# Optimization experiments

Measured on AMD Instinct MI355X. Metric: run time of the kernel, lower is better.

Reference implementation:

```python
import jax, jax.numpy as jnp
import numpy as np

UNITS = 1024
D_MODEL = 1024
H = 16
DK = 64
DV = 64
M = 128
B = 4
S = 1024


def setup_inputs() -> dict:
    key = jax.random.key(0)
    ks = jax.random.split(key, 12)
    s = 1.0 / np.sqrt(D_MODEL)
    inp = {
        "queries": jax.random.normal(ks[0], (B, S, D_MODEL), jnp.float32),
        "keys": jax.random.normal(ks[1], (B, S, D_MODEL), jnp.float32),
        "values": jax.random.normal(ks[2], (B, S, D_MODEL), jnp.float32),
        "Wq": jax.random.normal(ks[3], (D_MODEL, H * DK), jnp.float32) * s,
        "bq": jnp.zeros((H * DK,), jnp.float32),
        "Wk": jax.random.normal(ks[4], (D_MODEL, H * DK), jnp.float32) * s,
        "bk": jnp.zeros((H * DK,), jnp.float32),
        "Wv": jax.random.normal(ks[5], (D_MODEL, H * DV), jnp.float32) * s,
        "bv": jnp.zeros((H * DV,), jnp.float32),
        "Wo": jax.random.normal(ks[6], (H * DV, UNITS), jnp.float32) * (1.0 / np.sqrt(H * DV)),
        "bo": jnp.zeros((UNITS,), jnp.float32),
        "mk": jax.random.normal(ks[7], (1, M, H * DK), jnp.float32) * 0.1,
        "mv": jax.random.normal(ks[8], (1, M, H * DV), jnp.float32) * 0.1,
        "h": H,
    }
    return inp


def reference(queries, keys, values, Wq, bq, Wk, bk, Wv, bv, Wo, bo, mk, mv, h):
    Bq, Sq, _ = queries.shape
    m = mk.shape[1]
    dk = Wk.shape[1] // h
    dv = Wv.shape[1] // h
    scale_m = jnp.sqrt(jnp.asarray(m, queries.dtype))

    # Q projection: [B, h, Sq, dk]
    q = (queries @ Wq + bq).reshape(Bq, Sq, h, dk).transpose(0, 2, 1, 3)

    # K/V projections with m learned memory slots concatenated on the seq axis
    k_flat = jnp.concatenate(
        [keys @ Wk + bk, scale_m * jnp.broadcast_to(mk, (Bq, m, h * dk))], axis=1
    )  # [B, Sk+m, h*dk]
    v_flat = jnp.concatenate(
        [values @ Wv + bv, scale_m * jnp.broadcast_to(mv, (Bq, m, h * dv))], axis=1
    )  # [B, Sk+m, h*dv]
    Skm = k_flat.shape[1]
    k = k_flat.reshape(Bq, Skm, h, dk).transpose(0, 2, 1, 3)  # [B, h, Sk+m, dk]
    v = v_flat.reshape(Bq, Skm, h, dv).transpose(0, 2, 1, 3)  # [B, h, Sk+m, dv]

    # Scaled dot-product attention over sequence + memory slots
    scores = jnp.einsum("bhqd,bhkd->bhqk", q, k) / jnp.sqrt(jnp.asarray(dk, q.dtype))
    attn = jax.nn.softmax(scores, axis=-1)  # [B, h, Sq, Sk+m]
    out = jnp.einsum("bhqk,bhkd->bhqd", attn, v)  # [B, h, Sq, dv]
    out = out.transpose(0, 2, 1, 3).reshape(Bq, Sq, h * dv)
    return out @ Wo + bo
```

## Files before the change

kernel.cpp:

```cpp
#include <hip/hip_runtime.h>

typedef __attribute__((ext_vector_type(8))) __bf16 bf16x8;
typedef __attribute__((ext_vector_type(4))) float f32x4;

#define DEVINL __device__ __forceinline__

constexpr int BZ = 4;
constexpr int SEQ = 1024;
constexpr int DMODEL = 1024;
constexpr int NH = 16;
constexpr int HD = 64;
constexpr int MSLOT = 128;
constexpr int NT = BZ * SEQ;
constexpr int SKM = SEQ + MSLOT;
constexpr int VT_LD = BZ * SKM;
constexpr float SCALE_M = 11.313708498984761f;
constexpr float SCEXP = 0.18033688011112042f;
constexpr size_t OF_QIN  = 0;
constexpr size_t OF_KIN  = OF_QIN  + (size_t)NT * DMODEL;
constexpr size_t OF_VIN  = OF_KIN  + (size_t)NT * DMODEL;
constexpr size_t OF_WQT  = OF_VIN  + (size_t)NT * DMODEL;
constexpr size_t OF_WKT  = OF_WQT  + (size_t)DMODEL * DMODEL;
constexpr size_t OF_WVT  = OF_WKT  + (size_t)DMODEL * DMODEL;
constexpr size_t OF_WOT  = OF_WVT  + (size_t)DMODEL * DMODEL;
constexpr size_t OF_QB   = OF_WOT  + (size_t)DMODEL * DMODEL;
constexpr size_t OF_KPR  = OF_QB   + (size_t)NT * DMODEL;
constexpr size_t OF_KMEM = OF_KPR  + (size_t)NT * DMODEL;
constexpr size_t OF_VTG  = OF_KMEM + (size_t)MSLOT * DMODEL;
constexpr size_t OF_AOUT = OF_VTG  + (size_t)DMODEL * VT_LD;

DEVINL unsigned short f2bf(float f) {
  union { float f; unsigned u; } v; v.f = f;
  unsigned r = v.u + 0x7FFF + ((v.u >> 16) & 1);
  return (unsigned short)(r >> 16);
}

#if __has_builtin(__builtin_amdgcn_cvt_pk_bf16_f32)
DEVINL unsigned pack2(float a, float b) {
  auto t = __builtin_amdgcn_cvt_pk_bf16_f32(a, b);
  unsigned r; __builtin_memcpy(&r, &t, 4); return r;
}
#else
DEVINL unsigned pack2(float a, float b) {
  return (unsigned)f2bf(a) | ((unsigned)f2bf(b) << 16);
}
#endif

#if __has_builtin(__builtin_amdgcn_exp2f)
DEVINL float fast_exp2(float x) { return __builtin_amdgcn_exp2f(x); }
#else
DEVINL float fast_exp2(float x) { return exp2f(x); }
#endif

DEVINL f32x4 mfma16(bf16x8 a, bf16x8 b, f32x4 c) {
  return __builtin_amdgcn_mfma_f32_16x16x32_bf16(a, b, c, 0, 0, 0);
}

DEVINL void gload16(const unsigned short* gp, unsigned short* lp) {
  __builtin_amdgcn_global_load_lds(
      (const __attribute__((address_space(1))) unsigned int*)(const void*)gp,
      (__attribute__((address_space(3))) unsigned int*)(void*)lp, 16, 0, 0);
}

__global__ __launch_bounds__(256) void prep_all(
    const float* __restrict__ q, const float* __restrict__ k, const float* __restrict__ v,
    const float* __restrict__ W0, const float* __restrict__ W1,
    const float* __restrict__ W2, const float* __restrict__ W3,
    const float* __restrict__ mk, const float* __restrict__ mv,
    unsigned short* __restrict__ dq, unsigned short* __restrict__ dk,
    unsigned short* __restrict__ dv,
    unsigned short* __restrict__ d0, unsigned short* __restrict__ d1,
    unsigned short* __restrict__ d2, unsigned short* __restrict__ d3,
    unsigned short* __restrict__ Kmm, unsigned short* __restrict__ VtG) {
  __shared__ float t[32][65];
  const int tid = threadIdx.x;
  const int bid = blockIdx.x;
  if (bid < 6144) {
    const int tz = bid >> 11;
    const float* src = (tz == 0) ? q : (tz == 1) ? k : v;
    unsigned short* dst = (tz == 0) ? dq : (tz == 1) ? dk : dv;
    int i = ((bid & 2047) * 256 + tid) * 8;
    float4 v0 = *(const float4*)(src + i);
    float4 v1 = *(const float4*)(src + i + 4);
    union { unsigned u2[4]; uint4 v; } o;
    o.u2[0] = pack2(v0.x, v0.y); o.u2[1] = pack2(v0.z, v0.w);
    o.u2[2] = pack2(v1.x, v1.y); o.u2[3] = pack2(v1.z, v1.w);
    *(uint4*)(dst + i) = o.v;
  } else if (bid < 8192) {
    const int rel = bid - 6144;
    const int z = rel >> 9, rem = rel & 511;
    const float* src = (z == 0) ? W0 : (z == 1) ? W1 : (z == 2) ? W2 : W3;
    unsigned short* dst = (z == 0) ? d0 : (z == 1) ? d1 : (z == 2) ? d2 : d3;
    const int n0 = (rem & 31) * 32, k0 = (rem >> 5) * 64;
    {
      int c = tid & 31, rg = tid >> 5;
#pragma unroll
      for (int rr = 0; rr < 8; ++rr)
        t[c][rg * 8 + rr] = src[(size_t)(k0 + rg * 8 + rr) * DMODEL + n0 + c];
    }
    __syncthreads();
    {
      int n = tid >> 3, ck = tid & 7;
      union { unsigned short u[8]; uint4 v; } o;
#pragma unroll
      for (int j = 0; j < 8; ++j) o.u[j] = f2bf(t[n][ck * 8 + j]);
      *(uint4*)(dst + (size_t)(n0 + n) * DMODEL + k0 + ck * 8) = o.v;
    }
  } else if (bid < 8704) {
    int i = (bid - 8192) * 256 + tid;
    Kmm[i] = f2bf(mk[i] * SCALE_M);
  } else {
    const int rel = bid - 8704;
    const int j0 = (rel & 3) * 32, c0 = (rel >> 2) * 32;
    const int tx = tid & 31, ty = tid >> 5;
#pragma unroll
    for (int r = 0; r < 4; ++r)
      t[ty + r * 8][tx] = mv[(size_t)(j0 + ty + r * 8) * DMODEL + c0 + tx];
    __syncthreads();
#pragma unroll
    for (int r = 0; r < 4; ++r) {
      int c = c0 + ty + r * 8;
      unsigned short vv = f2bf(t[tx][ty + r * 8] * SCALE_M);
#pragma unroll
      for (int bb = 0; bb < BZ; ++bb)
        VtG[(size_t)c * VT_LD + bb * SKM + SEQ + j0 + tx] = vv;
    }
  }
}

__global__ __launch_bounds__(256, 3) void proj_qkv(
    const unsigned short* __restrict__ Qin, const unsigned short* __restrict__ Kin,
    const unsigned short* __restrict__ Vin, const unsigned short* __restrict__ Wqt,
    const unsigned short* __restrict__ Wkt, const unsigned short* __restrict__ Wvt,
    const float* __restrict__ bq, const float* __restrict__ bk,
    const float* __restrict__ bv, unsigned short* __restrict__ Qbp,
    unsigned short* __restrict__ Kprp, unsigned short* __restrict__ VtG) {
  __shared__ unsigned short As0[128 * 32], As1[128 * 32];
  __shared__ unsigned short Bs0[128 * 32], Bs1[128 * 32];
  const int tid = threadIdx.x;
  const int pid = blockIdx.x >> 8;
  const int idx = blockIdx.x & 255;
  const int w = tid >> 6, lane = tid & 63, quad = lane >> 4, l16 = lane & 15;
  const int wr = w >> 1, wc = w & 1;
  const int mt = idx & 31, nt = idx >> 5;
  f32x4 acc[4][4] = {};

  const unsigned short* Abase;
  const unsigned short* Bbase;
  if (pid == 0)      { Abase = Qin + (size_t)(mt * 128) * DMODEL; Bbase = Wqt + (size_t)(nt * 128) * DMODEL; }
  else if (pid == 1) { Abase = Kin + (size_t)(mt * 128) * DMODEL; Bbase = Wkt + (size_t)(nt * 128) * DMODEL; }
  else               { Abase = Wvt + (size_t)(nt * 128) * DMODEL; Bbase = Vin + (size_t)(mt * 128) * DMODEL; }

  for (int kt = 0; kt < 16; ++kt) {
    const int k0 = kt * 64;
#pragma unroll
    for (int hb = 0; hb < 2; ++hb) {
      unsigned short* al = hb ? As1 : As0;
      unsigned short* bl = hb ? Bs1 : Bs0;
#pragma unroll
      for (int gi = 0; gi < 2; ++gi) {
        int g = gi * 256 + tid;
        int row = g >> 2, slot = g & 3;
        gload16(Abase + (size_t)row * DMODEL + k0 + hb * 32 + slot * 8, al + g * 8);
        gload16(Bbase + (size_t)row * DMODEL + k0 + hb * 32 + slot * 8, bl + g * 8);
      }
    }
    __syncthreads();
#pragma unroll
    for (int hb = 0; hb < 2; ++hb) {
      const unsigned short* al = hb ? As1 : As0;
      const unsigned short* bl = hb ? Bs1 : Bs0;
      bf16x8 af[4], bfr[4];
#pragma unroll
      for (int rb = 0; rb < 4; ++rb)
        af[rb] = *(const bf16x8*)(al + (wr * 64 + rb * 16 + l16) * 32 + quad * 8);
#pragma unroll
      for (int cb = 0; cb < 4; ++cb)
        bfr[cb] = *(const bf16x8*)(bl + (wc * 64 + cb * 16 + l16) * 32 + quad * 8);
#pragma unroll
      for (int rb = 0; rb < 4; ++rb)
#pragma unroll
        for (int cb = 0; cb < 4; ++cb)
          acc[rb][cb] = mfma16(af[rb], bfr[cb], acc[rb][cb]);
    }
    __syncthreads();
  }

  if (pid < 2) {
    const float* bias   = pid ? bk : bq;
    unsigned short* out = pid ? Kprp : Qbp;
    const float osc     = pid ? 1.0f : SCEXP;
    const int m0 = mt * 128, n0 = nt * 128;
#pragma unroll
    for (int rb = 0; rb < 4; ++rb)
#pragma unroll
      for (int cb = 0; cb < 4; ++cb)
#pragma unroll
        for (int r = 0; r < 4; ++r) {
          int row = m0 + wr * 64 + rb * 16 + quad * 4 + r;
          int col = n0 + wc * 64 + cb * 16 + l16;
          out[(size_t)row * DMODEL + col] = f2bf((acc[rb][cb][r] + bias[col]) * osc);
        }
  } else {
    const int t0 = mt * 128, n0 = nt * 128;
#pragma unroll
    for (int rb = 0; rb < 4; ++rb)
#pragma unroll
      for (int cb = 0; cb < 4; ++cb)
#pragma unroll
        for (int r = 0; r < 4; ++r) {
          int n = n0 + wr * 64 + rb * 16 + quad * 4 + r;
          int tok = t0 + wc * 64 + cb * 16 + l16;
          int col = tok + (tok >> 10) * MSLOT;
          VtG[(size_t)n * VT_LD + col] = f2bf(acc[rb][cb][r] + bv[n]);
        }
  }
}

__global__ __launch_bounds__(256) void gemm_out(const unsigned short* __restrict__ A,
                                                const unsigned short* __restrict__ Wt,
                                                const float* __restrict__ bias,
                                                float* __restrict__ Cout) {
  __shared__ unsigned short As0[128 * 32], As1[128 * 32];
  __shared__ unsigned short Bs0[64 * 32], Bs1[64 * 32];
  const int tid = threadIdx.x;
  const int idx = blockIdx.x;
  const int mt = idx & 31, nt = idx >> 5;
  const int m0 = mt * 128, n0 = nt * 64;
  const int w = tid >> 6, lane = tid & 63, quad = lane >> 4, l16 = lane & 15;
  const int wr = w >> 1, wc = w & 1;
  f32x4 acc[4][2] = {};
  const unsigned short* Abase = A + (size_t)m0 * DMODEL;
  const unsigned short* Bbase = Wt + (size_t)n0 * DMODEL;

  for (int kt = 0; kt < 16; ++kt) {
    const int k0 = kt * 64;
#pragma unroll
    for (int hb = 0; hb < 2; ++hb) {
      unsigned short* al = hb ? As1 : As0;
#pragma unroll
      for (int gi = 0; gi < 2; ++gi) {
        int g = gi * 256 + tid;
        int row = g >> 2, slot = g & 3;
        gload16(Abase + (size_t)row * DMODEL + k0 + hb * 32 + slot * 8, al + g * 8);
      }
      unsigned short* bl = hb ? Bs1 : Bs0;
      int row = tid >> 2, slot = tid & 3;
      gload16(Bbase + (size_t)row * DMODEL + k0 + hb * 32 + slot * 8, bl + tid * 8);
    }
    __syncthreads();
#pragma unroll
    for (int hb = 0; hb < 2; ++hb) {
      const unsigned short* al = hb ? As1 : As0;
      const unsigned short* bl = hb ? Bs1 : Bs0;
      bf16x8 af[4], bfr[2];
#pragma unroll
      for (int rb = 0; rb < 4; ++rb)
        af[rb] = *(const bf16x8*)(al + (wr * 64 + rb * 16 + l16) * 32 + quad * 8);
#pragma unroll
      for (int cb = 0; cb < 2; ++cb)
        bfr[cb] = *(const bf16x8*)(bl + (wc * 32 + cb * 16 + l16) * 32 + quad * 8);
#pragma unroll
      for (int rb = 0; rb < 4; ++rb)
#pragma unroll
        for (int cb = 0; cb < 2; ++cb)
          acc[rb][cb] = mfma16(af[rb], bfr[cb], acc[rb][cb]);
    }
    __syncthreads();
  }
#pragma unroll
  for (int rb = 0; rb < 4; ++rb)
#pragma unroll
    for (int cb = 0; cb < 2; ++cb)
#pragma unroll
      for (int r = 0; r < 4; ++r) {
        int row = m0 + wr * 64 + rb * 16 + quad * 4 + r;
        int col = n0 + wc * 32 + cb * 16 + l16;
        Cout[(size_t)row * DMODEL + col] = acc[rb][cb][r] + bias[col];
      }
}

__global__ __launch_bounds__(256) void attn_kernel(const unsigned short* __restrict__ Qb,
                                                   const unsigned short* __restrict__ Kproj,
                                                   const unsigned short* __restrict__ Kmem,
                                                   const unsigned short* __restrict__ VtG,
                                                   unsigned short* __restrict__ Aout) {
  __shared__ unsigned short Ks[2][64 * 64];
  __shared__ unsigned short Vs[2][64 * 64];
  const int tid = threadIdx.x;
  const int bh = blockIdx.x & 63, qb = blockIdx.x >> 6;
  const int b = bh & 3, h = bh >> 2;
  const int w = tid >> 6, lane = tid & 63, quad = lane >> 4, l16 = lane & 15;
  const int token0 = b * SEQ + qb * 64 + w * 16;
  const int lx = l16 & 7;

  const int ck0 = 2 * w, ck1 = 2 * w + 1;
  const int lrow = lane >> 3;
  const int lslot = (lane & 7) ^ lrow;
  const int R0 = 8 * ck0 + lrow, R1 = 8 * ck1 + lrow;
  auto sig_inv = [](int R) {
    return (R & 0x20) | ((R & 0x0C) << 1) | ((R & 0x10) >> 2) | (R & 3);
  };
  const size_t ksrc0 = (size_t)sig_inv(R0) * DMODEL + lslot * 8;
  const size_t ksrc1 = (size_t)sig_inv(R1) * DMODEL + lslot * 8;
  const size_t vsrc0 = (size_t)R0 * VT_LD + lslot * 8;
  const size_t vsrc1 = (size_t)R1 * VT_LD + lslot * 8;
  const int ldst0 = ck0 * 512 + lane * 8;
  const int ldst1 = ck1 * 512 + lane * 8;

  auto kbase = [&](int tile) -> const unsigned short* {
    return (tile < 16) ? Kproj + (size_t)(b * SEQ + tile * 64) * DMODEL + h * HD
                       : Kmem + (size_t)((tile - 16) * 64) * DMODEL + h * HD;
  };
  auto vbase = [&](int tile) -> const unsigned short* {
    int c0 = (tile < 16) ? b * SKM + tile * 64 : b * SKM + SEQ + (tile - 16) * 64;
    return VtG + (size_t)(h * HD) * VT_LD + c0;
  };

  auto stage = [&](int buf, int tile) {
    const unsigned short* kp = kbase(tile);
    const unsigned short* vp = vbase(tile);
    gload16(kp + ksrc0, Ks[buf] + ldst0);
    gload16(kp + ksrc1, Ks[buf] + ldst1);
    gload16(vp + vsrc0, Vs[buf] + ldst0);
    gload16(vp + vsrc1, Vs[buf] + ldst1);
  };

  bf16x8 qf[2];
#pragma unroll
  for (int t = 0; t < 2; ++t)
    qf[t] = *(const bf16x8*)(Qb + (size_t)(token0 + l16) * DMODEL + h * HD + t * 32 + quad * 8);

  bf16x8 ones;
  {
    union { unsigned short u[8]; bf16x8 v; } one8;
#pragma unroll
    for (int i = 0; i < 8; ++i) one8.u[i] = 0x3F80;
    ones = one8.v;
  }

  f32x4 O[4] = {};
  f32x4 Lacc = {};

  auto tilecomp = [&](const unsigned short* Kbuf, const unsigned short* Vbuf) {
    f32x4 sc[4] = {};
    __builtin_amdgcn_s_setprio(1);
#pragma unroll
    for (int c = 0; c < 4; ++c)
#pragma unroll
      for (int t = 0; t < 2; ++t) {
        bf16x8 kb = *(const bf16x8*)(Kbuf + (c * 16 + l16) * 64 +
                                     ((t * 4 + quad) ^ lx) * 8);
        sc[c] = mfma16(kb, qf[t], sc[c]);
      }
    __builtin_amdgcn_s_setprio(0);

    float e[4][4];
#pragma unroll
    for (int c = 0; c < 4; ++c)
#pragma unroll
      for (int r = 0; r < 4; ++r)
        e[c][r] = fast_exp2(sc[c][r]);

    __builtin_amdgcn_s_setprio(1);
#pragma unroll
    for (int t2 = 0; t2 < 2; ++t2) {
      union { unsigned u[4]; bf16x8 v; } pa;
      pa.u[0] = pack2(e[2 * t2][0],     e[2 * t2][1]);
      pa.u[1] = pack2(e[2 * t2][2],     e[2 * t2][3]);
      pa.u[2] = pack2(e[2 * t2 + 1][0], e[2 * t2 + 1][1]);
      pa.u[3] = pack2(e[2 * t2 + 1][2], e[2 * t2 + 1][3]);
      Lacc = mfma16(pa.v, ones, Lacc);
#pragma unroll
      for (int c2 = 0; c2 < 4; ++c2) {
        bf16x8 vb = *(const bf16x8*)(Vbuf + (c2 * 16 + l16) * 64 +
                                     ((t2 * 4 + quad) ^ lx) * 8);
        O[c2] = mfma16(pa.v, vb, O[c2]);
      }
    }
    __builtin_amdgcn_s_setprio(0);
  };

  stage(0, 0);
  __syncthreads();

  for (int p = 0; p < 9; ++p) {
    stage(1, 2 * p + 1);
    tilecomp(Ks[0], Vs[0]);
    __syncthreads();
    if (p < 8) stage(0, 2 * p + 2);
    tilecomp(Ks[1], Vs[1]);
    __syncthreads();
  }

#pragma unroll
  for (int r = 0; r < 4; ++r) {
    float inv = 1.0f / Lacc[r];
#pragma unroll
    for (int c2 = 0; c2 < 4; ++c2)
      Aout[(size_t)(token0 + quad * 4 + r) * DMODEL + h * HD + c2 * 16 + l16] =
          f2bf(O[c2][r] * inv);
  }
}

extern "C" void kernel_launch(void* const* d_in, const int* in_sizes, int n_in,
                              void* d_out, int out_size, void* d_ws, size_t ws_size,
                              hipStream_t stream) {
  const float* queries = (const float*)d_in[0];
  const float* keys    = (const float*)d_in[1];
  const float* values  = (const float*)d_in[2];
  const float* Wq = (const float*)d_in[3];
  const float* bq = (const float*)d_in[4];
  const float* Wk = (const float*)d_in[5];
  const float* bk = (const float*)d_in[6];
  const float* Wv = (const float*)d_in[7];
  const float* bv = (const float*)d_in[8];
  const float* Wo = (const float*)d_in[9];
  const float* bo = (const float*)d_in[10];
  const float* mk = (const float*)d_in[11];
  const float* mv = (const float*)d_in[12];

  unsigned short* ws = (unsigned short*)d_ws;
  unsigned short* Qin  = ws + OF_QIN;
  unsigned short* Kin  = ws + OF_KIN;
  unsigned short* Vin  = ws + OF_VIN;
  unsigned short* Wqt  = ws + OF_WQT;
  unsigned short* Wkt  = ws + OF_WKT;
  unsigned short* Wvt  = ws + OF_WVT;
  unsigned short* Wot  = ws + OF_WOT;
  unsigned short* Qbp  = ws + OF_QB;
  unsigned short* Kprp = ws + OF_KPR;
  unsigned short* Kmm  = ws + OF_KMEM;
  unsigned short* VtGp = ws + OF_VTG;
  unsigned short* Aoutp = ws + OF_AOUT;

  prep_all<<<8832, 256, 0, stream>>>(queries, keys, values, Wq, Wk, Wv, Wo, mk, mv,
                                     Qin, Kin, Vin, Wqt, Wkt, Wvt, Wot, Kmm, VtGp);

  proj_qkv<<<768, 256, 0, stream>>>(Qin, Kin, Vin, Wqt, Wkt, Wvt, bq, bk, bv,
                                    Qbp, Kprp, VtGp);

  attn_kernel<<<1024, 256, 0, stream>>>(Qbp, Kprp, Kmm, VtGp, Aoutp);

  gemm_out<<<512, 256, 0, stream>>>(Aoutp, Wot, bo, (float*)d_out);
}
```

Baseline: 204.5 us.

## Switch attention kernel to 32x32x16 MFMA with key-split warps and LDS reduction

Rewrites the attention inner loop to use 32x32x16 bf16 MFMA instead of 16x16x32. Each warp now owns 32 queries and half of the 64-key tile, so two warps split the keys and their partial outputs and row sums are merged through shared memory at the end. The row sum is now a plain register add instead of an extra MFMA against a ones vector. The K-load swizzle permutation changes to match the new fragment layout, and the final store writes packed bf16 pairs. The cost is an extra LDS reduction and barrier in the epilogue, plus larger accumulators that raise register pressure.

```diff
diff --git a/kernel.cpp b/kernel.cpp
--- a/kernel.cpp
+++ b/kernel.cpp
@@ -2,6 +2,7 @@
 
 typedef __attribute__((ext_vector_type(8))) __bf16 bf16x8;
 typedef __attribute__((ext_vector_type(4))) float f32x4;
+typedef __attribute__((ext_vector_type(16))) float f32x16;
 
 #define DEVINL __device__ __forceinline__
 
@@ -54,6 +55,9 @@
 
 DEVINL f32x4 mfma16(bf16x8 a, bf16x8 b, f32x4 c) {
   return __builtin_amdgcn_mfma_f32_16x16x32_bf16(a, b, c, 0, 0, 0);
+}
+DEVINL f32x16 mfma32(bf16x8 a, bf16x8 b, f32x16 c) {
+  return __builtin_amdgcn_mfma_f32_32x32x16_bf16(a, b, c, 0, 0, 0);
 }
 
 DEVINL void gload16(const unsigned short* gp, unsigned short* lp) {
@@ -290,16 +294,19 @@
   const int tid = threadIdx.x;
   const int bh = blockIdx.x & 63, qb = blockIdx.x >> 6;
   const int b = bh & 3, h = bh >> 2;
-  const int w = tid >> 6, lane = tid & 63, quad = lane >> 4, l16 = lane & 15;
-  const int token0 = b * SEQ + qb * 64 + w * 16;
-  const int lx = l16 & 7;
+  const int w = tid >> 6, lane = tid & 63;
+  const int l32 = lane & 31, hi = lane >> 5;
+  const int qw = (w & 1) * 32;
+  const int kh = (w >> 1) * 32;
+  const int tokq = b * SEQ + qb * 64 + qw + l32;
+  const int lx7 = l32 & 7;
 
   const int ck0 = 2 * w, ck1 = 2 * w + 1;
   const int lrow = lane >> 3;
   const int lslot = (lane & 7) ^ lrow;
   const int R0 = 8 * ck0 + lrow, R1 = 8 * ck1 + lrow;
   auto sig_inv = [](int R) {
-    return (R & 0x20) | ((R & 0x0C) << 1) | ((R & 0x10) >> 2) | (R & 3);
+    return (R & ~0xC) | ((R & 4) << 1) | ((R & 8) >> 1);
   };
   const size_t ksrc0 = (size_t)sig_inv(R0) * DMODEL + lslot * 8;
   const size_t ksrc1 = (size_t)sig_inv(R1) * DMODEL + lslot * 8;
@@ -326,57 +333,44 @@
     gload16(vp + vsrc1, Vs[buf] + ldst1);
   };
 
-  bf16x8 qf[2];
-#pragma unroll
-  for (int t = 0; t < 2; ++t)
-    qf[t] = *(const bf16x8*)(Qb + (size_t)(token0 + l16) * DMODEL + h * HD + t * 32 + quad * 8);
-
-  bf16x8 ones;
-  {
-    union { unsigned short u[8]; bf16x8 v; } one8;
-#pragma unroll
-    for (int i = 0; i < 8; ++i) one8.u[i] = 0x3F80;
-    ones = one8.v;
-  }
-
-  f32x4 O[4] = {};
-  f32x4 Lacc = {};
+  bf16x8 qf[4];
+#pragma unroll
+  for (int t = 0; t < 4; ++t)
+    qf[t] = *(const bf16x8*)(Qb + (size_t)tokq * DMODEL + h * HD + t * 16 + hi * 8);
+
+  f32x16 Oa = {}, Ob = {};
+  float Lp = 0.0f;
 
   auto tilecomp = [&](const unsigned short* Kbuf, const unsigned short* Vbuf) {
-    f32x4 sc[4] = {};
+    f32x16 sc = {};
     __builtin_amdgcn_s_setprio(1);
 #pragma unroll
-    for (int c = 0; c < 4; ++c)
-#pragma unroll
-      for (int t = 0; t < 2; ++t) {
-        bf16x8 kb = *(const bf16x8*)(Kbuf + (c * 16 + l16) * 64 +
-                                     ((t * 4 + quad) ^ lx) * 8);
-        sc[c] = mfma16(kb, qf[t], sc[c]);
-      }
+    for (int t = 0; t < 4; ++t) {
+      bf16x8 kb = *(const bf16x8*)(Kbuf + (kh + l32) * 64 + ((2 * t + hi) ^ lx7) * 8);
+      sc = mfma32(kb, qf[t], sc);
+    }
     __builtin_amdgcn_s_setprio(0);
 
-    float e[4][4];
-#pragma unroll
-    for (int c = 0; c < 4; ++c)
-#pragma unroll
-      for (int r = 0; r < 4; ++r)
-        e[c][r] = fast_exp2(sc[c][r]);
+    float e[16];
+#pragma unroll
+    for (int r = 0; r < 16; ++r) e[r] = fast_exp2(sc[r]);
+#pragma unroll
+    for (int r = 0; r < 16; ++r) Lp += e[r];
 
     __builtin_amdgcn_s_setprio(1);
 #pragma unroll
-    for (int t2 = 0; t2 < 2; ++t2) {
+    for (int s = 0; s < 2; ++s) {
       union { unsigned u[4]; bf16x8 v; } pa;
-      pa.u[0] = pack2(e[2 * t2][0],     e[2 * t2][1]);
-      pa.u[1] = pack2(e[2 * t2][2],     e[2 * t2][3]);
-      pa.u[2] = pack2(e[2 * t2 + 1][0], e[2 * t2 + 1][1]);
-      pa.u[3] = pack2(e[2 * t2 + 1][2], e[2 * t2 + 1][3]);
-      Lacc = mfma16(pa.v, ones, Lacc);
-#pragma unroll
-      for (int c2 = 0; c2 < 4; ++c2) {
-        bf16x8 vb = *(const bf16x8*)(Vbuf + (c2 * 16 + l16) * 64 +
-                                     ((t2 * 4 + quad) ^ lx) * 8);
-        O[c2] = mfma16(pa.v, vb, O[c2]);
-      }
+      pa.u[0] = pack2(e[8 * s + 0], e[8 * s + 1]);
+      pa.u[1] = pack2(e[8 * s + 2], e[8 * s + 3]);
+      pa.u[2] = pack2(e[8 * s + 4], e[8 * s + 5]);
+      pa.u[3] = pack2(e[8 * s + 6], e[8 * s + 7]);
+      bf16x8 vb0 = *(const bf16x8*)(Vbuf + l32 * 64 +
+                                    (((kh >> 3) + 2 * s + hi) ^ lx7) * 8);
+      Oa = mfma32(vb0, pa.v, Oa);
+      bf16x8 vb1 = *(const bf16x8*)(Vbuf + (32 + l32) * 64 +
+                                    (((kh >> 3) + 2 * s + hi) ^ lx7) * 8);
+      Ob = mfma32(vb1, pa.v, Ob);
     }
     __builtin_amdgcn_s_setprio(0);
   };
@@ -393,13 +387,37 @@
     __syncthreads();
   }
 
-#pragma unroll
-  for (int r = 0; r < 4; ++r) {
-    float inv = 1.0f / Lacc[r];
-#pragma unroll
-    for (int c2 = 0; c2 < 4; ++c2)
-      Aout[(size_t)(token0 + quad * 4 + r) * DMODEL + h * HD + c2 * 16 + l16] =
-          f2bf(O[c2][r] * inv);
+  float* obuf = (float*)(&Ks[0][0]);
+  float* lbuf = (float*)(&Vs[0][0]);
+  if (w >= 2) {
+#pragma unroll
+    for (int r = 0; r < 16; ++r) {
+      obuf[r * 128 + (w - 2) * 64 + lane] = Oa[r];
+      obuf[(16 + r) * 128 + (w - 2) * 64 + lane] = Ob[r];
+    }
+    lbuf[(w - 2) * 64 + lane] = Lp;
+  }
+  __syncthreads();
+  if (w < 2) {
+#pragma unroll
+    for (int r = 0; r < 16; ++r) {
+      Oa[r] += obuf[r * 128 + w * 64 + lane];
+      Ob[r] += obuf[(16 + r) * 128 + w * 64 + lane];
+    }
+    Lp += lbuf[w * 64 + lane];
+    float Lfull = Lp + __shfl_xor(Lp, 32, 64);
+    float inv = 1.0f / Lfull;
+    unsigned short* orow = Aout + (size_t)tokq * DMODEL + h * HD;
+#pragma unroll
+    for (int a = 0; a < 4; ++a) {
+      uint2 pk0, pk1;
+      pk0.x = pack2(Oa[4 * a + 0] * inv, Oa[4 * a + 1] * inv);
+      pk0.y = pack2(Oa[4 * a + 2] * inv, Oa[4 * a + 3] * inv);
+      *(uint2*)(orow + 8 * a + 4 * hi) = pk0;
+      pk1.x = pack2(Ob[4 * a + 0] * inv, Ob[4 * a + 1] * inv);
+      pk1.y = pack2(Ob[4 * a + 2] * inv, Ob[4 * a + 3] * inv);
+      *(uint2*)(orow + 32 + 8 * a + 4 * hi) = pk1;
+    }
   }
 }
 
```

New measurement: 208.7 us. 1.02x slower.
